# Kernel optimization log

Measured on AMD Instinct MI355X. Metric: run time of the kernel, lower is better.

The kernel has to match this reference:

```python
import jax, jax.numpy as jnp
import numpy as np

N_EMBD = 1024
N_HEADS = 16
HEAD_DIM = N_EMBD // N_HEADS


def setup_inputs() -> dict:
    key = jax.random.key(0)
    ks = jax.random.split(key, 5)
    s = 0.02
    return {
        "x": jax.random.normal(ks[0], (4, 2048, N_EMBD), dtype=jnp.float32),
        "w_attn": jax.random.normal(ks[1], (N_EMBD, 3 * N_EMBD), dtype=jnp.float32) * s,
        "b_attn": jnp.zeros((3 * N_EMBD,), dtype=jnp.float32),
        "w_proj": jax.random.normal(ks[2], (N_EMBD, N_EMBD), dtype=jnp.float32) * s,
        "b_proj": jnp.zeros((N_EMBD,), dtype=jnp.float32),
    }


def reference(x, w_attn, b_attn, w_proj, b_proj):
    B, T, C = x.shape
    H, D = N_HEADS, HEAD_DIM
    qkv = x @ w_attn + b_attn                      # [B,T,3C]
    q, k, v = jnp.split(qkv, 3, axis=-1)
    q = q.reshape(B, T, H, D).transpose(0, 2, 1, 3)  # [B,H,T,D]
    k = k.reshape(B, T, H, D).transpose(0, 2, 1, 3)
    v = v.reshape(B, T, H, D).transpose(0, 2, 1, 3)
    # Faithful to source bug: divide by d**(-0.5) == multiply by sqrt(d)
    scale = jnp.asarray(D, x.dtype) ** 0.5
    scores = jnp.einsum("bhqd,bhkd->bhqk", q, k) * scale  # [B,H,T,T]
    causal = jnp.tril(jnp.ones((T, T), dtype=bool))
    scores = jnp.where(causal[None, None], scores, -jnp.inf)
    attn = jax.nn.softmax(scores, axis=-1)
    y = jnp.einsum("bhqk,bhkd->bhqd", attn, v)     # [B,H,T,D]
    y = y.transpose(0, 2, 1, 3).reshape(B, T, C)
    return y @ w_proj + b_proj
```

## Files before the change

kernel.cpp:

```cpp
#include <hip/hip_runtime.h>
#include <cmath>

#define BB 4
#define TT 2048
#define CC 1024
#define HH 16
#define DD 64
#define MM (BB*TT)

typedef _Float16 f16x8 __attribute__((ext_vector_type(8)));
typedef _Float16 f16x4 __attribute__((ext_vector_type(4)));
typedef _Float16 f16x2 __attribute__((ext_vector_type(2)));
typedef float f32x4 __attribute__((ext_vector_type(4)));
typedef unsigned short ushort_t;

#define MFMA16(a,b,c) __builtin_amdgcn_mfma_f32_16x16x16f16(a,b,c,0,0,0)

__device__ __forceinline__ unsigned short f2h(float f) {
    _Float16 h = (_Float16)f;
    return __builtin_bit_cast(unsigned short, h);
}

__device__ __forceinline__ f16x2 cvt_pk(float a, float b) {
    return __builtin_bit_cast(f16x2, __builtin_amdgcn_cvt_pkrtz(a, b));
}

__device__ __forceinline__ void gld16(const void* gsrc, void* ldst) {
    void* g = const_cast<void*>(gsrc);
    __builtin_amdgcn_global_load_lds(
        (__attribute__((address_space(1))) void*)g,
        (__attribute__((address_space(3))) void*)ldst,
        16, 0, 0);
}

__global__ __launch_bounds__(256)
void cvt4_kernel(const float* __restrict__ in, ushort_t* __restrict__ out, long n4) {
    long i = (long)blockIdx.x * blockDim.x + threadIdx.x;
    if (i >= n4) return;
    float4 v = ((const float4*)in)[i];
    ushort4 o;
    o.x = f2h(v.x); o.y = f2h(v.y); o.z = f2h(v.z); o.w = f2h(v.w);
    ((ushort4*)out)[i] = o;
}

__global__ __launch_bounds__(256)
void trcvt_kernel(const float* __restrict__ in, ushort_t* __restrict__ out,
                  int K, int N) {
    __shared__ float T[32][33];
    const int tx = threadIdx.x & 31;
    const int ty = threadIdx.x >> 5;
    const int n0 = blockIdx.x * 32;
    const int k0 = blockIdx.y * 32;
    #pragma unroll
    for (int i = 0; i < 4; ++i)
        T[ty + i * 8][tx] = in[(size_t)(k0 + ty + i * 8) * N + n0 + tx];
    __syncthreads();
    #pragma unroll
    for (int i = 0; i < 4; ++i)
        out[(size_t)(n0 + ty + i * 8) * K + k0 + tx] = f2h(T[tx][ty + i * 8]);
}

template<int BM, int NN, bool QKV>
__global__ __launch_bounds__(512, 2)
void hgemm2_kernel(const ushort_t* __restrict__ A, const ushort_t* __restrict__ Bt,
                   const float* __restrict__ bias, float* __restrict__ out,
                   ushort_t* __restrict__ qh, ushort_t* __restrict__ kh,
                   ushort_t* __restrict__ vh)
{
    constexpr int K    = 1024;
    constexpr int MT   = BM / 32;
    constexpr int AJ   = BM / 128;
    constexpr int AH   = BM * 32;
    constexpr int BH   = 256 * 32;
    constexpr int SLOT = AH + BH;
    extern __shared__ ushort_t LDS[];

    const int tid  = threadIdx.x;
    const int lane = tid & 63;
    const int wid  = tid >> 6;
    const int wm   = wid >> 2;
    const int wn   = wid & 3;
    const int lrow = lane & 15;
    const int quad = lane >> 4;
    const int m0   = blockIdx.y * BM;
    const int n0   = blockIdx.x * 256;

    const int lsw   = (lane * 16) ^ ((lane & 32) ? 32 : 0);
    const int rowin = lsw >> 6;
    const int scolh = (lsw & 63) >> 1;
    unsigned voffA[AJ], voffB[2];
    #pragma unroll
    for (int j = 0; j < AJ; ++j)
        voffA[j] = (unsigned)(m0 + (j * 8 + wid) * 16 + rowin) * K + scolh;
    #pragma unroll
    for (int j = 0; j < 2; ++j)
        voffB[j] = (unsigned)(n0 + (j * 8 + wid) * 16 + rowin) * K + scolh;
    const int ldsW = wid * 512;
    const int rdo = (lrow * 32 + quad * 8) ^ ((lrow & 8) ? 16 : 0);

    f32x4 acc[MT][4];
    const f32x4 z = {0.f, 0.f, 0.f, 0.f};
    #pragma unroll
    for (int mt = 0; mt < MT; ++mt)
        #pragma unroll
        for (int nt = 0; nt < 4; ++nt)
            acc[mt][nt] = z;

    auto STAGE = [&](int kt) {
        ushort_t* sb = &LDS[(kt & 3) * SLOT];
        #pragma unroll
        for (int j = 0; j < AJ; ++j)
            gld16(A + voffA[j] + kt * 32, sb + j * 4096 + ldsW);
        #pragma unroll
        for (int j = 0; j < 2; ++j)
            gld16(Bt + voffB[j] + kt * 32, sb + AH + j * 4096 + ldsW);
    };
    auto COMPUTE = [&](int kt) {
        const ushort_t* As = &LDS[(kt & 3) * SLOT];
        const ushort_t* Bs = As + AH;
        f16x8 af[MT], bf[4];
        #pragma unroll
        for (int mt = 0; mt < MT; ++mt)
            af[mt] = *(const f16x8*)&As[(wm * MT + mt) * 512 + rdo];
        #pragma unroll
        for (int nt = 0; nt < 4; ++nt)
            bf[nt] = *(const f16x8*)&Bs[(wn * 4 + nt) * 512 + rdo];
        __builtin_amdgcn_s_setprio(1);
        #pragma unroll
        for (int mt = 0; mt < MT; ++mt)
            #pragma unroll
            for (int nt = 0; nt < 4; ++nt)
                acc[mt][nt] = __builtin_amdgcn_mfma_f32_16x16x32_f16(
                    af[mt], bf[nt], acc[mt][nt], 0, 0, 0);
        __builtin_amdgcn_s_setprio(0);
    };

    STAGE(0);
    STAGE(1);
    for (int kt = 0; kt < 31; ++kt) {
        if constexpr (BM == 256)
            asm volatile("s_waitcnt vmcnt(4)" ::: "memory");
        else
            asm volatile("s_waitcnt vmcnt(3)" ::: "memory");
        __builtin_amdgcn_s_barrier();
        if (kt < 30) STAGE(kt + 2);
        COMPUTE(kt);
    }
    asm volatile("s_waitcnt vmcnt(0)" ::: "memory");
    __builtin_amdgcn_s_barrier();
    COMPUTE(31);

    #pragma unroll
    for (int mt = 0; mt < MT; ++mt) {
        const int rbase = m0 + wm * (BM / 2) + mt * 16 + quad * 4;
        #pragma unroll
        for (int nt = 0; nt < 4; ++nt) {
            const int col = n0 + wn * 64 + nt * 16 + lrow;
            const float bv = bias[col];
            if (QKV) {
                const int which = col >> 10;
                const int c = col & 1023;
                const int h = c >> 6, d = c & 63;
                const int b = rbase >> 11, t0 = rbase & 2047;
                if (which == 2) {
                    ushort4 pk;
                    pk.x = f2h(acc[mt][nt][0] + bv);
                    pk.y = f2h(acc[mt][nt][1] + bv);
                    pk.z = f2h(acc[mt][nt][2] + bv);
                    pk.w = f2h(acc[mt][nt][3] + bv);
                    *(ushort4*)&vh[(((size_t)b * HH + h) * DD + d) * TT + t0] = pk;
                } else {
                    ushort_t* dst = which ? kh : qh;
                    const float sc = which ? 1.0f : 8.0f * 1.44269504088896f;
                    #pragma unroll
                    for (int r = 0; r < 4; ++r)
                        dst[(((size_t)b * HH + h) * TT + t0 + r) * DD + d] =
                            f2h((acc[mt][nt][r] + bv) * sc);
                }
            } else {
                #pragma unroll
                for (int r = 0; r < 4; ++r)
                    out[(size_t)(rbase + r) * NN + col] = acc[mt][nt][r] + bv;
            }
        }
    }
}

__global__ __launch_bounds__(256, 4)
void attn_mfma_kernel(const ushort_t* __restrict__ qh, const ushort_t* __restrict__ kh,
                      const ushort_t* __restrict__ vh, ushort_t* __restrict__ yh)
{
    __shared__ ushort_t Ks[2][64 * 72];
    __shared__ ushort_t Vs[2][64 * 72];

    const int pr   = blockIdx.x;
    const int bh   = blockIdx.y;
    const int qtA  = 31 - pr;
    const int qtB  = pr;
    const int tid  = threadIdx.x;
    const int lane = tid & 63;
    const int w    = tid >> 6;
    const int lrow = lane & 15;
    const int quad = lane >> 4;

    const ushort_t* qbase = qh + (size_t)bh * TT * DD;
    const ushort_t* kbase = kh + (size_t)bh * TT * DD;
    const ushort_t* vbase = vh + (size_t)bh * DD * TT;
    const int b = bh >> 4, h = bh & 15;

    const int ur = tid >> 3;
    const int uc = (tid & 7) * 8;

    int q0w = qtA * 64 + w * 16;
    f16x8 aq0 = *(const f16x8*)&qbase[(size_t)(q0w + lrow) * DD + quad * 8];
    f16x8 aq1 = *(const f16x8*)&qbase[(size_t)(q0w + lrow) * DD + 32 + quad * 8];

    const f32x4 z = {0.f, 0.f, 0.f, 0.f};
    f32x4 o[4] = {z, z, z, z};
    float mi = -1e30f, li = 0.f;

    uint4 kr0 = *(const uint4*)&kbase[(size_t)ur * DD + uc];
    uint4 kr1 = *(const uint4*)&kbase[(size_t)(ur + 32) * DD + uc];
    uint4 vr0 = *(const uint4*)&vbase[(size_t)ur * TT + uc];
    uint4 vr1 = *(const uint4*)&vbase[(size_t)(ur + 32) * TT + uc];

    *(uint4*)&Ks[0][(ur)      * 72 + uc] = kr0;
    *(uint4*)&Ks[0][(ur + 32) * 72 + uc] = kr1;
    *(uint4*)&Vs[0][(ur)      * 72 + uc] = vr0;
    *(uint4*)&Vs[0][(ur + 32) * 72 + uc] = vr1;
    {
        const int nkt = (1 <= qtA) ? 1 : 0;
        const int nb  = nkt * 64;
        kr0 = *(const uint4*)&kbase[(size_t)(nb + ur) * DD + uc];
        kr1 = *(const uint4*)&kbase[(size_t)(nb + ur + 32) * DD + uc];
        vr0 = *(const uint4*)&vbase[(size_t)ur * TT + nb + uc];
        vr1 = *(const uint4*)&vbase[(size_t)(ur + 32) * TT + nb + uc];
    }
    __syncthreads();

    for (int i = 0; i <= 32; ++i) {
        const int cur = i & 1;
        if (i == qtA + 1) {
            #pragma unroll
            for (int r = 0; r < 4; ++r) {
                const float inv = 1.0f / __shfl(li, quad * 4 + r, 64);
                const int t = q0w + quad * 4 + r;
                #pragma unroll
                for (int dt = 0; dt < 4; ++dt)
                    yh[((size_t)b * TT + t) * CC + h * 64 + dt * 16 + lrow] =
                        f2h(o[dt][r] * inv);
            }
            q0w = qtB * 64 + w * 16;
            aq0 = *(const f16x8*)&qbase[(size_t)(q0w + lrow) * DD + quad * 8];
            aq1 = *(const f16x8*)&qbase[(size_t)(q0w + lrow) * DD + 32 + quad * 8];
            #pragma unroll
            for (int dt = 0; dt < 4; ++dt) o[dt] = z;
            mi = -1e30f; li = 0.f;
        }
        const int kt = (i <= qtA) ? i : i - qtA - 1;

        f32x4 sv[4];
        __builtin_amdgcn_s_setprio(1);
        #pragma unroll
        for (int c = 0; c < 4; ++c) {
            f16x8 ka = *(const f16x8*)&Ks[cur][(c * 16 + lrow) * 72 + quad * 8];
            f16x8 kb = *(const f16x8*)&Ks[cur][(c * 16 + lrow) * 72 + 32 + quad * 8];
            sv[c] = __builtin_amdgcn_mfma_f32_16x16x32_f16(ka, aq0, z, 0, 0, 0);
            sv[c] = __builtin_amdgcn_mfma_f32_16x16x32_f16(kb, aq1, sv[c], 0, 0, 0);
        }
        __builtin_amdgcn_s_setprio(0);

        const int kt2 = kt * 64;
        const int qg  = q0w + lrow;
        const bool diag = (i == qtA) || (i == 32);
        if (diag) {
            #pragma unroll
            for (int c = 0; c < 4; ++c)
                #pragma unroll
                for (int r = 0; r < 4; ++r)
                    if (kt2 + c * 16 + quad * 4 + r > qg) sv[c][r] = -3e38f;
        }
        float mc[4];
        #pragma unroll
        for (int c = 0; c < 4; ++c)
            mc[c] = fmaxf(fmaxf(sv[c][0], sv[c][1]), fmaxf(sv[c][2], sv[c][3]));
        float m = fmaxf(fmaxf(mc[0], mc[1]), fmaxf(mc[2], mc[3]));
        m = fmaxf(m, __shfl_xor(m, 16, 64));
        m = fmaxf(m, __shfl_xor(m, 32, 64));

        if (__any(m > mi + 8.0f)) {
            const float mnew  = fmaxf(mi, m);
            const float alpha = exp2f(mi - mnew);
            mi = mnew;
            li *= alpha;
            #pragma unroll
            for (int r = 0; r < 4; ++r) {
                const float ar = __shfl(alpha, quad * 4 + r, 64);
                #pragma unroll
                for (int dt = 0; dt < 4; ++dt) o[dt][r] *= ar;
            }
        }

        f16x4 ap[4];
        float rc[4];
        #pragma unroll
        for (int c = 0; c < 4; ++c) {
            const float p0 = exp2f(sv[c][0] - mi);
            const float p1 = exp2f(sv[c][1] - mi);
            const float p2 = exp2f(sv[c][2] - mi);
            const float p3 = exp2f(sv[c][3] - mi);
            rc[c] = (p0 + p1) + (p2 + p3);
            const f16x2 lo = cvt_pk(p0, p1);
            const f16x2 hi = cvt_pk(p2, p3);
            ap[c][0] = lo[0]; ap[c][1] = lo[1]; ap[c][2] = hi[0]; ap[c][3] = hi[1];
        }
        float rs = (rc[0] + rc[1]) + (rc[2] + rc[3]);
        rs += __shfl_xor(rs, 16, 64);
        rs += __shfl_xor(rs, 32, 64);
        li += rs;

        __builtin_amdgcn_s_setprio(1);
        #pragma unroll
        for (int dt = 0; dt < 4; ++dt)
            #pragma unroll
            for (int c = 0; c < 4; ++c) {
                f16x4 vb = *(const f16x4*)&Vs[cur][(dt * 16 + lrow) * 72 + c * 16 + quad * 4];
                o[dt] = MFMA16(ap[c], vb, o[dt]);
            }
        __builtin_amdgcn_s_setprio(0);

        if (i < 32) {
            const int nxt = cur ^ 1;
            *(uint4*)&Ks[nxt][(ur)      * 72 + uc] = kr0;
            *(uint4*)&Ks[nxt][(ur + 32) * 72 + uc] = kr1;
            *(uint4*)&Vs[nxt][(ur)      * 72 + uc] = vr0;
            *(uint4*)&Vs[nxt][(ur + 32) * 72 + uc] = vr1;
            if (i < 31) {
                const int ni  = i + 2;
                const int nkt = (ni <= qtA) ? ni : ni - qtA - 1;
                const int nb  = nkt * 64;
                kr0 = *(const uint4*)&kbase[(size_t)(nb + ur) * DD + uc];
                kr1 = *(const uint4*)&kbase[(size_t)(nb + ur + 32) * DD + uc];
                vr0 = *(const uint4*)&vbase[(size_t)ur * TT + nb + uc];
                vr1 = *(const uint4*)&vbase[(size_t)(ur + 32) * TT + nb + uc];
            }
        }
        __syncthreads();
    }

    #pragma unroll
    for (int r = 0; r < 4; ++r) {
        const float inv = 1.0f / __shfl(li, quad * 4 + r, 64);
        const int t = q0w + quad * 4 + r;
        #pragma unroll
        for (int dt = 0; dt < 4; ++dt)
            yh[((size_t)b * TT + t) * CC + h * 64 + dt * 16 + lrow] =
                f2h(o[dt][r] * inv);
    }
}

extern "C" void kernel_launch(void* const* d_in, const int* in_sizes, int n_in,
                              void* d_out, int out_size, void* d_ws, size_t ws_size,
                              hipStream_t stream) {
    const float* x      = (const float*)d_in[0];
    const float* w_attn = (const float*)d_in[1];
    const float* b_attn = (const float*)d_in[2];
    const float* w_proj = (const float*)d_in[3];
    const float* b_proj = (const float*)d_in[4];
    float* out = (float*)d_out;

    const size_t per = (size_t)BB * HH * TT * DD;
    ushort_t* qh  = (ushort_t*)d_ws;
    ushort_t* kh  = qh + per;
    ushort_t* vh  = kh + per;
    ushort_t* xh  = vh + per;
    ushort_t* yh  = xh;
    ushort_t* wat = xh + (size_t)MM * CC;
    ushort_t* wpt = wat + (size_t)3 * CC * CC;

    cvt4_kernel<<<(MM * CC / 4 + 255) / 256, 256, 0, stream>>>(x, xh, MM * CC / 4);
    trcvt_kernel<<<dim3(3 * CC / 32, CC / 32), 256, 0, stream>>>(w_attn, wat, CC, 3 * CC);
    trcvt_kernel<<<dim3(CC / 32, CC / 32), 256, 0, stream>>>(w_proj, wpt, CC, CC);

    hgemm2_kernel<256, 3 * CC, true>
        <<<dim3(3 * CC / 256, MM / 256), 512, 4 * (256 * 32 + 256 * 32) * 2, stream>>>(
        xh, wat, b_attn, nullptr, qh, kh, vh);

    attn_mfma_kernel<<<dim3(16, BB * HH), 256, 0, stream>>>(qh, kh, vh, yh);

    hgemm2_kernel<128, CC, false>
        <<<dim3(CC / 256, MM / 128), 512, 4 * (128 * 32 + 256 * 32) * 2, stream>>>(
        yh, wpt, b_proj, out, nullptr, nullptr, nullptr);
}
```

Before: 280.1 us.

## Retile GEMMs, add block swizzle, 3-stage LDS ring, and LDS-staged V transpose

Generalizes the GEMM kernel over BM/BN and the warp layout. QKV now uses 128x256 tiles and the output projection uses 128x128 tiles, giving more blocks on the device. Adds an XCD-aware block-index swizzle and switches from a 4-slot to a 3-slot LDS ring buffer with plain unswizzled LDS addressing. V outputs are transposed through LDS so stores to the transposed V layout are coalesced 16-byte writes. Removing the XOR swizzle on LDS reads may add bank conflicts, and dropping the launch-bounds occupancy hint changes register allocation.

```diff
diff --git a/kernel.cpp b/kernel.cpp
--- a/kernel.cpp
+++ b/kernel.cpp
@@ -60,123 +60,156 @@
         out[(size_t)(n0 + ty + i * 8) * K + k0 + tx] = f2h(T[tx][ty + i * 8]);
 }
 
-template<int BM, int NN, bool QKV>
-__global__ __launch_bounds__(512, 2)
+template<int BM, int BN, int WN, int NN, bool QKV>
+__global__ __launch_bounds__(512)
 void hgemm2_kernel(const ushort_t* __restrict__ A, const ushort_t* __restrict__ Bt,
                    const float* __restrict__ bias, float* __restrict__ out,
                    ushort_t* __restrict__ qh, ushort_t* __restrict__ kh,
                    ushort_t* __restrict__ vh)
 {
     constexpr int K    = 1024;
-    constexpr int MT   = BM / 32;
-    constexpr int AJ   = BM / 128;
+    constexpr int WM   = 8 / WN;
+    constexpr int MT   = BM / WM / 16;
+    constexpr int NT   = BN / WN / 16;
+    constexpr int LA   = BM / 128;
+    constexpr int LB   = BN / 128;
+    constexpr int NLD  = LA + LB;
     constexpr int AH   = BM * 32;
-    constexpr int BH   = 256 * 32;
+    constexpr int BH   = BN * 32;
     constexpr int SLOT = AH + BH;
     extern __shared__ ushort_t LDS[];
 
     const int tid  = threadIdx.x;
     const int lane = tid & 63;
     const int wid  = tid >> 6;
-    const int wm   = wid >> 2;
-    const int wn   = wid & 3;
+    const int wm   = wid / WN;
+    const int wn   = wid % WN;
     const int lrow = lane & 15;
     const int quad = lane >> 4;
-    const int m0   = blockIdx.y * BM;
-    const int n0   = blockIdx.x * 256;
-
-    const int lsw   = (lane * 16) ^ ((lane & 32) ? 32 : 0);
-    const int rowin = lsw >> 6;
-    const int scolh = (lsw & 63) >> 1;
-    unsigned voffA[AJ], voffB[2];
-    #pragma unroll
-    for (int j = 0; j < AJ; ++j)
-        voffA[j] = (unsigned)(m0 + (j * 8 + wid) * 16 + rowin) * K + scolh;
-    #pragma unroll
-    for (int j = 0; j < 2; ++j)
-        voffB[j] = (unsigned)(n0 + (j * 8 + wid) * 16 + rowin) * K + scolh;
-    const int ldsW = wid * 512;
-    const int rdo = (lrow * 32 + quad * 8) ^ ((lrow & 8) ? 16 : 0);
-
-    f32x4 acc[MT][4];
+
+    const int gx  = gridDim.x;
+    const int nwg = gx * gridDim.y;
+    int bid = blockIdx.y * gx + blockIdx.x;
+    bid = (bid & 7) * (nwg >> 3) + (bid >> 3);
+    const int m0 = (bid / gx) * BM;
+    const int n0 = (bid % gx) * BN;
+
+    const int srow  = lane >> 2;
+    const int scolh = (lane & 3) * 8;
+    unsigned voffA[LA], voffB[LB];
+    #pragma unroll
+    for (int j = 0; j < LA; ++j)
+        voffA[j] = (unsigned)(m0 + (j * 8 + wid) * 16 + srow) * K + scolh;
+    #pragma unroll
+    for (int j = 0; j < LB; ++j)
+        voffB[j] = (unsigned)(n0 + (j * 8 + wid) * 16 + srow) * K + scolh;
+
+    f32x4 acc[MT][NT];
     const f32x4 z = {0.f, 0.f, 0.f, 0.f};
     #pragma unroll
     for (int mt = 0; mt < MT; ++mt)
         #pragma unroll
-        for (int nt = 0; nt < 4; ++nt)
+        for (int nt = 0; nt < NT; ++nt)
             acc[mt][nt] = z;
 
-    auto STAGE = [&](int kt) {
-        ushort_t* sb = &LDS[(kt & 3) * SLOT];
-        #pragma unroll
-        for (int j = 0; j < AJ; ++j)
-            gld16(A + voffA[j] + kt * 32, sb + j * 4096 + ldsW);
-        #pragma unroll
-        for (int j = 0; j < 2; ++j)
-            gld16(Bt + voffB[j] + kt * 32, sb + AH + j * 4096 + ldsW);
+    auto STAGE = [&](int kt, int ss) {
+        ushort_t* sb = &LDS[ss * SLOT];
+        #pragma unroll
+        for (int j = 0; j < LA; ++j)
+            gld16(A + voffA[j] + kt * 32, sb + (j * 8 + wid) * 512);
+        #pragma unroll
+        for (int j = 0; j < LB; ++j)
+            gld16(Bt + voffB[j] + kt * 32, sb + AH + (j * 8 + wid) * 512);
     };
-    auto COMPUTE = [&](int kt) {
-        const ushort_t* As = &LDS[(kt & 3) * SLOT];
+    auto COMPUTE = [&](int cs) {
+        const ushort_t* As = &LDS[cs * SLOT];
         const ushort_t* Bs = As + AH;
-        f16x8 af[MT], bf[4];
+        f16x8 af[MT], bf[NT];
         #pragma unroll
         for (int mt = 0; mt < MT; ++mt)
-            af[mt] = *(const f16x8*)&As[(wm * MT + mt) * 512 + rdo];
-        #pragma unroll
-        for (int nt = 0; nt < 4; ++nt)
-            bf[nt] = *(const f16x8*)&Bs[(wn * 4 + nt) * 512 + rdo];
+            af[mt] = *(const f16x8*)&As[(wm * MT + mt) * 512 + lrow * 32 + quad * 8];
+        #pragma unroll
+        for (int nt = 0; nt < NT; ++nt)
+            bf[nt] = *(const f16x8*)&Bs[(wn * NT + nt) * 512 + lrow * 32 + quad * 8];
         __builtin_amdgcn_s_setprio(1);
         #pragma unroll
         for (int mt = 0; mt < MT; ++mt)
             #pragma unroll
-            for (int nt = 0; nt < 4; ++nt)
+            for (int nt = 0; nt < NT; ++nt)
                 acc[mt][nt] = __builtin_amdgcn_mfma_f32_16x16x32_f16(
                     af[mt], bf[nt], acc[mt][nt], 0, 0, 0);
         __builtin_amdgcn_s_setprio(0);
     };
 
-    STAGE(0);
-    STAGE(1);
+    STAGE(0, 0);
+    STAGE(1, 1);
+    int cs = 0;
     for (int kt = 0; kt < 31; ++kt) {
-        if constexpr (BM == 256)
-            asm volatile("s_waitcnt vmcnt(4)" ::: "memory");
+        if constexpr (NLD == 3)
+            asm volatile("s_waitcnt vmcnt(3)" ::: "memory");
         else
-            asm volatile("s_waitcnt vmcnt(3)" ::: "memory");
+            asm volatile("s_waitcnt vmcnt(2)" ::: "memory");
         __builtin_amdgcn_s_barrier();
-        if (kt < 30) STAGE(kt + 2);
-        COMPUTE(kt);
+        if (kt < 30) STAGE(kt + 2, cs == 0 ? 2 : cs - 1);
+        COMPUTE(cs);
+        cs = (cs == 2) ? 0 : cs + 1;
     }
     asm volatile("s_waitcnt vmcnt(0)" ::: "memory");
     __builtin_amdgcn_s_barrier();
-    COMPUTE(31);
+    COMPUTE(cs);
+
+    if (QKV && (n0 >> 10) == 2) {
+        __syncthreads();
+        ushort_t* Tr = &LDS[0];
+        #pragma unroll
+        for (int mt = 0; mt < MT; ++mt) {
+            const int tl = wm * (BM / WM) + mt * 16 + quad * 4;
+            #pragma unroll
+            for (int nt = 0; nt < NT; ++nt) {
+                const int cl = wn * (BN / WN) + nt * 16 + lrow;
+                const float bv = bias[n0 + cl];
+                ushort4 pk;
+                pk.x = f2h(acc[mt][nt][0] + bv);
+                pk.y = f2h(acc[mt][nt][1] + bv);
+                pk.z = f2h(acc[mt][nt][2] + bv);
+                pk.w = f2h(acc[mt][nt][3] + bv);
+                *(ushort4*)&Tr[cl * 136 + tl] = pk;
+            }
+        }
+        __syncthreads();
+        const int v0  = n0 & 1023;
+        const int b2  = m0 >> 11;
+        const int t0b = m0 & 2047;
+        const int ch  = (tid & 15) * 8;
+        #pragma unroll
+        for (int it = 0; it < 8; ++it) {
+            const int c  = it * 32 + (tid >> 4);
+            const int dg = v0 + c;
+            const uint4 val = *(const uint4*)&Tr[c * 136 + ch];
+            *(uint4*)&vh[(((size_t)b2 * HH + (dg >> 6)) * DD + (dg & 63)) * TT
+                         + t0b + ch] = val;
+        }
+        return;
+    }
 
     #pragma unroll
     for (int mt = 0; mt < MT; ++mt) {
-        const int rbase = m0 + wm * (BM / 2) + mt * 16 + quad * 4;
-        #pragma unroll
-        for (int nt = 0; nt < 4; ++nt) {
-            const int col = n0 + wn * 64 + nt * 16 + lrow;
+        const int rbase = m0 + wm * (BM / WM) + mt * 16 + quad * 4;
+        #pragma unroll
+        for (int nt = 0; nt < NT; ++nt) {
+            const int col = n0 + wn * (BN / WN) + nt * 16 + lrow;
             const float bv = bias[col];
             if (QKV) {
                 const int which = col >> 10;
                 const int c = col & 1023;
                 const int h = c >> 6, d = c & 63;
                 const int b = rbase >> 11, t0 = rbase & 2047;
-                if (which == 2) {
-                    ushort4 pk;
-                    pk.x = f2h(acc[mt][nt][0] + bv);
-                    pk.y = f2h(acc[mt][nt][1] + bv);
-                    pk.z = f2h(acc[mt][nt][2] + bv);
-                    pk.w = f2h(acc[mt][nt][3] + bv);
-                    *(ushort4*)&vh[(((size_t)b * HH + h) * DD + d) * TT + t0] = pk;
-                } else {
-                    ushort_t* dst = which ? kh : qh;
-                    const float sc = which ? 1.0f : 8.0f * 1.44269504088896f;
-                    #pragma unroll
-                    for (int r = 0; r < 4; ++r)
-                        dst[(((size_t)b * HH + h) * TT + t0 + r) * DD + d] =
-                            f2h((acc[mt][nt][r] + bv) * sc);
-                }
+                ushort_t* dst = which ? kh : qh;
+                const float sc = which ? 1.0f : 8.0f * 1.44269504088896f;
+                #pragma unroll
+                for (int r = 0; r < 4; ++r)
+                    dst[(((size_t)b * HH + h) * TT + t0 + r) * DD + d] =
+                        f2h((acc[mt][nt][r] + bv) * sc);
             } else {
                 #pragma unroll
                 for (int r = 0; r < 4; ++r)
@@ -382,13 +415,13 @@
     trcvt_kernel<<<dim3(3 * CC / 32, CC / 32), 256, 0, stream>>>(w_attn, wat, CC, 3 * CC);
     trcvt_kernel<<<dim3(CC / 32, CC / 32), 256, 0, stream>>>(w_proj, wpt, CC, CC);
 
-    hgemm2_kernel<256, 3 * CC, true>
-        <<<dim3(3 * CC / 256, MM / 256), 512, 4 * (256 * 32 + 256 * 32) * 2, stream>>>(
+    hgemm2_kernel<128, 256, 4, 3 * CC, true>
+        <<<dim3(3 * CC / 256, MM / 128), 512, 73728, stream>>>(
         xh, wat, b_attn, nullptr, qh, kh, vh);
 
     attn_mfma_kernel<<<dim3(16, BB * HH), 256, 0, stream>>>(qh, kh, vh, yh);
 
-    hgemm2_kernel<128, CC, false>
-        <<<dim3(CC / 256, MM / 128), 512, 4 * (128 * 32 + 256 * 32) * 2, stream>>>(
+    hgemm2_kernel<128, 128, 2, CC, false>
+        <<<dim3(CC / 128, MM / 128), 512, 49152, stream>>>(
         yh, wpt, b_proj, out, nullptr, nullptr, nullptr);
 }
```

Result: slower. 287.6 us (+2.7%).
